# Optimization experiments

Hardware: AMD Instinct MI355X
Metric: run time of the kernel (lower is better)

## Reference

```python
import jax, jax.numpy as jnp
import numpy as np

N_NODES = 50000


def _graph_conv(x, src, dst, W, b):
    """DGL GraphConv with norm='both', bias, weight applied pre-aggregation.
    x: [N, Fin]; src/dst: [E] int; W: [Fin, Fout]; b: [Fout]."""
    N = x.shape[0]
    ones = jnp.ones(src.shape, jnp.float32)
    deg_out = jnp.maximum(jax.ops.segment_sum(ones, src, num_segments=N), 1.0)
    deg_in = jnp.maximum(jax.ops.segment_sum(ones, dst, num_segments=N), 1.0)
    h = (x * jax.lax.rsqrt(deg_out)[:, None]) @ W          # [N, Fout]
    m = jax.ops.segment_sum(h[src], dst, num_segments=N)   # SpMM aggregate
    return m * jax.lax.rsqrt(deg_in)[:, None] + b


def setup_inputs() -> dict:
    key = jax.random.key(0)
    ks = jax.random.split(key, 12)
    N = N_NODES
    e_sizes = {"rsr": 3000000, "rtr": 1000000, "rur": 200000}
    inp = {"x": jax.random.normal(ks[0], (N, 32), jnp.float32)}
    for i, (name, E) in enumerate(e_sizes.items()):
        inp[f"src_{name}"] = jax.random.randint(ks[1 + 2 * i], (E,), 0, N, jnp.int64)
        inp[f"dst_{name}"] = jax.random.randint(ks[2 + 2 * i], (E,), 0, N, jnp.int64)
    inp["W1"] = jax.random.normal(ks[7], (3, 32, 16), jnp.float32) / np.sqrt(32.0)
    inp["b1"] = jnp.zeros((3, 16), jnp.float32)
    inp["W2"] = jax.random.normal(ks[8], (3, 16, 1), jnp.float32) / np.sqrt(16.0)
    inp["b2"] = jnp.zeros((3, 1), jnp.float32)
    return inp


def reference(x, src_rsr, dst_rsr, src_rtr, dst_rtr, src_rur, dst_rur, W1, b1, W2, b2):
    edges = [(src_rsr, dst_rsr), (src_rtr, dst_rtr), (src_rur, dst_rur)]
    # layer 1: HeteroGraphConv(sum over relations) -> relu
    h = sum(_graph_conv(x, s, d, W1[r], b1[r]) for r, (s, d) in enumerate(edges))
    h = jax.nn.relu(h)
    # layer 2 -> squeeze
    out = sum(_graph_conv(h, s, d, W2[r], b2[r]) for r, (s, d) in enumerate(edges))
    return out[:, 0]
```

## Files before the change

### kernel.cpp

```cpp
#include <hip/hip_runtime.h>

#define N_NODES 50000
#define FH 16
#define NBUK 782
#define BSHIFT 6
#define BSTRIDE 800
#define TILE 4096
#define NCH2 64
#define NRNG 8
#define RNGSZ 6250
#define C1CAP 4608

#define OFF_INVOUT   0u
#define OFF_INVIN    150000u
#define OFF_BUKCNT   300000u
#define OFF_BSTART   302400u
#define OFF_GCUR     304800u
#define OFF_ROWPTR   307200u
#define OFF_HPROJ    457216u
#define OFF_HOUT     2857216u
#define OFF_AGGP     3657216u
#define OFF_SRCHIST  3657216u
#define OFF_HS       6057216u
#define OFF_OUTP     6207216u
#define OFF_PAIRS    6357216u
#define OFF_SRCSORT  10557216u

__global__ void k_zero_u32(unsigned* __restrict__ p, int n) {
    int i = blockIdx.x * 256 + threadIdx.x;
    if (i < n) p[i] = 0u;
}

__global__ __launch_bounds__(256) void k_srcDeg(const int* s0, const int* s1, const int* s2,
                                                int E0, int E1, int E2,
                                                unsigned* __restrict__ histP) {
    __shared__ unsigned bins[RNGSZ / 2];
    int c = blockIdx.x, rg = blockIdx.y, r = blockIdx.z;
    const int* arr = (r == 0) ? s0 : (r == 1) ? s1 : s2;
    int E = (r == 0) ? E0 : (r == 1) ? E1 : E2;
    for (int i = threadIdx.x; i < RNGSZ / 2; i += 256) bins[i] = 0u;
    __syncthreads();
    int lo = rg * RNGSZ;
    int per = (((E + NCH2 - 1) / NCH2) + 7) & ~7;
    int a0 = c * per, a1 = min(a0 + per, E);
    for (int i = a0 + (int)threadIdx.x * 8; i < a1; i += 2048) {
        if (i + 8 <= a1) {
            int4 v1 = *reinterpret_cast<const int4*>(arr + i);
            int4 v2 = *reinterpret_cast<const int4*>(arr + i + 4);
            unsigned d0 = (unsigned)(v1.x - lo), d1 = (unsigned)(v1.y - lo);
            unsigned d2 = (unsigned)(v1.z - lo), d3 = (unsigned)(v1.w - lo);
            unsigned d4 = (unsigned)(v2.x - lo), d5 = (unsigned)(v2.y - lo);
            unsigned d6 = (unsigned)(v2.z - lo), d7 = (unsigned)(v2.w - lo);
            if (d0 < (unsigned)RNGSZ) atomicAdd(&bins[d0 >> 1], (d0 & 1u) ? 65536u : 1u);
            if (d1 < (unsigned)RNGSZ) atomicAdd(&bins[d1 >> 1], (d1 & 1u) ? 65536u : 1u);
            if (d2 < (unsigned)RNGSZ) atomicAdd(&bins[d2 >> 1], (d2 & 1u) ? 65536u : 1u);
            if (d3 < (unsigned)RNGSZ) atomicAdd(&bins[d3 >> 1], (d3 & 1u) ? 65536u : 1u);
            if (d4 < (unsigned)RNGSZ) atomicAdd(&bins[d4 >> 1], (d4 & 1u) ? 65536u : 1u);
            if (d5 < (unsigned)RNGSZ) atomicAdd(&bins[d5 >> 1], (d5 & 1u) ? 65536u : 1u);
            if (d6 < (unsigned)RNGSZ) atomicAdd(&bins[d6 >> 1], (d6 & 1u) ? 65536u : 1u);
            if (d7 < (unsigned)RNGSZ) atomicAdd(&bins[d7 >> 1], (d7 & 1u) ? 65536u : 1u);
        } else {
            for (int k2 = i; k2 < a1; k2++) {
                unsigned d = (unsigned)(arr[k2] - lo);
                if (d < (unsigned)RNGSZ) atomicAdd(&bins[d >> 1], (d & 1u) ? 65536u : 1u);
            }
        }
    }
    __syncthreads();
    unsigned* out = histP + ((size_t)r * NCH2 + c) * 25000 + rg * (RNGSZ / 2);
    for (int i = threadIdx.x; i < RNGSZ / 2; i += 256) out[i] = bins[i];
}

__global__ void k_degreduceOut(const unsigned* __restrict__ histP, float* __restrict__ invOut) {
    int n = blockIdx.x * 256 + threadIdx.x;
    int r = blockIdx.y;
    if (n >= N_NODES) return;
    const unsigned* p = histP + (size_t)r * NCH2 * 25000 + (n >> 1);
    unsigned s = 0;
#pragma unroll
    for (int c = 0; c < NCH2; c++) {
        unsigned w = p[(size_t)c * 25000];
        s += (n & 1) ? (w >> 16) : (w & 0xFFFFu);
    }
    invOut[r * N_NODES + n] = rsqrtf((float)(s ? s : 1u));
}

__global__ __launch_bounds__(256) void k_bukCount(const int* d0p, const int* d1p, const int* d2p,
                                                  int E0, int E1, int E2,
                                                  unsigned* __restrict__ bukCnt) {
    __shared__ unsigned bins[NBUK];
    int c = blockIdx.x, r = blockIdx.y;
    const int* arr = (r == 0) ? d0p : (r == 1) ? d1p : d2p;
    int E = (r == 0) ? E0 : (r == 1) ? E1 : E2;
    for (int i = threadIdx.x; i < NBUK; i += 256) bins[i] = 0u;
    __syncthreads();
    int nb = gridDim.x;
    int per = (((E + nb - 1) / nb) + 3) & ~3;
    int a0 = c * per, a1 = min(a0 + per, E);
    for (int i = a0 + (int)threadIdx.x * 4; i < a1; i += 1024) {
        if (i + 4 <= a1) {
            int4 v = *reinterpret_cast<const int4*>(arr + i);
            atomicAdd(&bins[((unsigned)v.x) >> BSHIFT], 1u);
            atomicAdd(&bins[((unsigned)v.y) >> BSHIFT], 1u);
            atomicAdd(&bins[((unsigned)v.z) >> BSHIFT], 1u);
            atomicAdd(&bins[((unsigned)v.w) >> BSHIFT], 1u);
        } else {
            for (int k2 = i; k2 < a1; k2++)
                atomicAdd(&bins[((unsigned)arr[k2]) >> BSHIFT], 1u);
        }
    }
    __syncthreads();
    for (int b = threadIdx.x; b < NBUK; b += 256)
        if (bins[b]) atomicAdd(&bukCnt[r * BSTRIDE + b], bins[b]);
}

__global__ __launch_bounds__(256) void k_bucketScan(const unsigned* __restrict__ bukCnt,
                                                    unsigned* __restrict__ bstart,
                                                    unsigned* __restrict__ gcur) {
    __shared__ unsigned part[256];
    int r = blockIdx.x, t = threadIdx.x;
    unsigned loc[4]; unsigned s = 0;
#pragma unroll
    for (int k = 0; k < 4; k++) {
        int idx = 4 * t + k;
        loc[k] = (idx < NBUK) ? bukCnt[r * BSTRIDE + idx] : 0u;
        s += loc[k];
    }
    part[t] = s;
    __syncthreads();
    for (int d = 1; d < 256; d <<= 1) {
        unsigned v = (t >= d) ? part[t - d] : 0u;
        __syncthreads();
        part[t] += v;
        __syncthreads();
    }
    unsigned run = part[t] - s;
#pragma unroll
    for (int k = 0; k < 4; k++) {
        int idx = 4 * t + k;
        if (idx <= NBUK) { bstart[r * BSTRIDE + idx] = run; gcur[r * BSTRIDE + idx] = run; }
        run += loc[k];
    }
}

__global__ __launch_bounds__(256) void k_passB(
    const int* s0p, const int* s1p, const int* s2p,
    const int* d0p, const int* d1p, const int* d2p,
    int E0, int E1, int E2, int po0, int po1, int po2,
    unsigned* __restrict__ pairsAll, unsigned* __restrict__ gcurAll) {
    __shared__ unsigned cnt[NBUK];
    __shared__ unsigned off[NBUK];
    __shared__ unsigned gbase[NBUK];
    __shared__ unsigned part[256];
    __shared__ unsigned spair[TILE];
    __shared__ unsigned saddr[TILE];
    int r = blockIdx.z;
    const int* src = (r == 0) ? s0p : (r == 1) ? s1p : s2p;
    const int* dst = (r == 0) ? d0p : (r == 1) ? d1p : d2p;
    int E = (r == 0) ? E0 : (r == 1) ? E1 : E2;
    unsigned* pairs = pairsAll + ((r == 0) ? po0 : (r == 1) ? po1 : po2);
    unsigned* gcur = gcurAll + r * BSTRIDE;
    int nb = gridDim.x;
    int chunk = (((E + nb - 1) / nb) + 15) & ~15;
    int c0 = blockIdx.x * chunk;
    int c1 = min(c0 + chunk, E);
    for (int t0 = c0; t0 < c1; t0 += TILE) {
        int tn = min(TILE, c1 - t0);
        for (int i = threadIdx.x; i < NBUK; i += 256) cnt[i] = 0u;
        __syncthreads();
        unsigned pk[16], bk[16], sl[16];
        if (tn == TILE) {
            int base = t0 + (int)threadIdx.x * 16;
#pragma unroll
            for (int q = 0; q < 4; q++) {
                int4 vs = *reinterpret_cast<const int4*>(src + base + q * 4);
                int4 vd = *reinterpret_cast<const int4*>(dst + base + q * 4);
                pk[q * 4 + 0] = ((unsigned)vd.x << 16) | (unsigned)vs.x;
                pk[q * 4 + 1] = ((unsigned)vd.y << 16) | (unsigned)vs.y;
                pk[q * 4 + 2] = ((unsigned)vd.z << 16) | (unsigned)vs.z;
                pk[q * 4 + 3] = ((unsigned)vd.w << 16) | (unsigned)vs.w;
                bk[q * 4 + 0] = (unsigned)vd.x >> BSHIFT;
                bk[q * 4 + 1] = (unsigned)vd.y >> BSHIFT;
                bk[q * 4 + 2] = (unsigned)vd.z >> BSHIFT;
                bk[q * 4 + 3] = (unsigned)vd.w >> BSHIFT;
            }
#pragma unroll
            for (int k = 0; k < 16; k++) sl[k] = atomicAdd(&cnt[bk[k]], 1u);
        } else {
#pragma unroll
            for (int k = 0; k < 16; k++) {
                int ii = k * 256 + (int)threadIdx.x;
                bk[k] = 0xFFFFFFFFu;
                if (ii < tn) {
                    int i = t0 + ii;
                    unsigned s = (unsigned)src[i], d = (unsigned)dst[i];
                    pk[k] = (d << 16) | s;
                    unsigned b = d >> BSHIFT;
                    bk[k] = b;
                    sl[k] = atomicAdd(&cnt[b], 1u);
                }
            }
        }
        __syncthreads();
        {
            int t = threadIdx.x;
            unsigned loc[4]; unsigned sloc = 0;
#pragma unroll
            for (int k2 = 0; k2 < 4; k2++) {
                int idx = 4 * t + k2;
                loc[k2] = (idx < NBUK) ? cnt[idx] : 0u;
                sloc += loc[k2];
            }
            part[t] = sloc;
            __syncthreads();
            for (int d = 1; d < 256; d <<= 1) {
                unsigned v = (t >= d) ? part[t - d] : 0u;
                __syncthreads();
                part[t] += v;
                __syncthreads();
            }
            unsigned run = part[t] - sloc;
#pragma unroll
            for (int k2 = 0; k2 < 4; k2++) {
                int idx = 4 * t + k2;
                if (idx < NBUK) off[idx] = run;
                run += loc[k2];
            }
        }
        __syncthreads();
        for (int b = threadIdx.x; b < NBUK; b += 256) {
            unsigned c = cnt[b];
            if (c) gbase[b] = atomicAdd(&gcur[b], c);
        }
        __syncthreads();
        if (tn == TILE) {
#pragma unroll
            for (int k = 0; k < 16; k++) {
                unsigned idx = off[bk[k]] + sl[k];
                spair[idx] = pk[k];
                saddr[idx] = gbase[bk[k]] + sl[k];
            }
        } else {
#pragma unroll
            for (int k = 0; k < 16; k++) {
                if (bk[k] != 0xFFFFFFFFu) {
                    unsigned idx = off[bk[k]] + sl[k];
                    spair[idx] = pk[k];
                    saddr[idx] = gbase[bk[k]] + sl[k];
                }
            }
        }
        __syncthreads();
#pragma unroll
        for (int k = 0; k < 16; k++) {
            int ii = k * 256 + (int)threadIdx.x;
            if (ii < tn) pairs[saddr[ii]] = spair[ii];
        }
        __syncthreads();
    }
}

__global__ __launch_bounds__(256) void k_h1(const float* __restrict__ x, const float* __restrict__ invOut,
                                            const float* __restrict__ W1, float* __restrict__ hproj) {
    __shared__ float sW[32 * FH];
    __shared__ float sx[16][32];
    int r = blockIdx.y;
    const float* W = W1 + r * 32 * FH;
    int t = threadIdx.x;
    for (int i = t; i < 32 * FH; i += 256) sW[i] = W[i];
    int n0 = blockIdx.x * 16;
    for (int i = t; i < 16 * 32; i += 256) {
        int nn = i >> 5, kk = i & 31;
        int n = n0 + nn;
        sx[nn][kk] = (n < N_NODES) ? x[n * 32 + kk] : 0.0f;
    }
    __syncthreads();
    int nn = t >> 4, j = t & 15;
    int n = n0 + nn;
    if (n < N_NODES) {
        float s = 0.f;
#pragma unroll
        for (int k = 0; k < 32; k++) s += sx[nn][k] * sW[k * FH + j];
        hproj[((size_t)r * N_NODES + n) * FH + j] = s * invOut[r * N_NODES + n];
    }
}

__global__ __launch_bounds__(256) void k_passC1(
    const unsigned* __restrict__ pairsAll, int po1, int po2,
    const unsigned* __restrict__ bstartAll,
    const float4* __restrict__ h4All, float4* __restrict__ out4All,
    unsigned short* __restrict__ srcGAll, unsigned* __restrict__ rowptrAll,
    float* __restrict__ invInAll) {
    __shared__ unsigned cnt[64];
    __shared__ unsigned off[65];
    __shared__ unsigned cur[64];
    __shared__ unsigned short srcS[C1CAP];
    int b = blockIdx.x, t = threadIdx.x, r = blockIdx.z;
    int po = (r == 0) ? 0 : (r == 1) ? po1 : po2;
    const unsigned* pairs = pairsAll + po;
    const unsigned* bstart = bstartAll + r * BSTRIDE;
    const float4* h4 = h4All + (size_t)r * N_NODES * 4;
    float4* out4 = out4All + (size_t)r * N_NODES * 4;
    unsigned short* srcG = srcGAll + po;
    unsigned* rowptr = rowptrAll + (size_t)r * (N_NODES + 1);
    float* invIn = invInAll + (size_t)r * N_NODES;
    unsigned e0 = bstart[b], e1 = bstart[b + 1];
    if (e1 - e0 > (unsigned)C1CAP) e1 = e0 + (unsigned)C1CAP;
    int d0 = b << BSHIFT;
    if (t < 64) cnt[t] = 0u;
    __syncthreads();
    for (unsigned i = e0 + t; i < e1; i += 256)
        atomicAdd(&cnt[(pairs[i] >> 16) - (unsigned)d0], 1u);
    __syncthreads();
    if (t < 64) {
        unsigned cv = cnt[t];
        unsigned sc = cv;
#pragma unroll
        for (int d = 1; d < 64; d <<= 1) {
            unsigned v = __shfl_up(sc, d, 64);
            if (t >= d) sc += v;
        }
        off[t] = sc - cv;
        if (t == 63) off[64] = sc;
    }
    __syncthreads();
    if (t < 64) {
        cur[t] = off[t];
        int n = d0 + t;
        if (n < N_NODES) {
            rowptr[n] = (unsigned)po + e0 + off[t];
            unsigned dg = cnt[t];
            invIn[n] = rsqrtf((float)(dg ? dg : 1u));
        }
    }
    if (b == NBUK - 1 && t == 0) rowptr[N_NODES] = (unsigned)po + e1;
    __syncthreads();
    for (unsigned i = e0 + t; i < e1; i += 256) {
        unsigned p = pairs[i];
        unsigned d = (p >> 16) - (unsigned)d0;
        unsigned pos = atomicAdd(&cur[d], 1u);
        srcS[pos] = (unsigned short)(p & 0xFFFFu);
    }
    __syncthreads();
    {
        unsigned len = e1 - e0;
        for (unsigned i = t; i < len; i += 256) srcG[e0 + i] = srcS[i];
    }
    int unit = t >> 4, p = t & 15, k = p >> 2, fq = p & 3;
    for (int nd = unit; nd < 64; nd += 16) {
        unsigned o0 = off[nd], o1 = off[nd + 1];
        float ax = 0.f, ay = 0.f, az = 0.f, aw = 0.f;
        unsigned base = o0;
        for (; base + 8 <= o1; base += 8) {
            int s0 = srcS[base + k], s1 = srcS[base + 4 + k];
            float4 v0 = h4[(size_t)s0 * 4 + fq];
            float4 v1 = h4[(size_t)s1 * 4 + fq];
            ax += v0.x + v1.x; ay += v0.y + v1.y; az += v0.z + v1.z; aw += v0.w + v1.w;
        }
        for (; base < o1; base += 4) {
            unsigned idx = base + (unsigned)k;
            if (idx < o1) {
                int s = srcS[idx];
                float4 v = h4[(size_t)s * 4 + fq];
                ax += v.x; ay += v.y; az += v.z; aw += v.w;
            }
        }
        ax += __shfl_xor(ax, 4, 16); ay += __shfl_xor(ay, 4, 16);
        az += __shfl_xor(az, 4, 16); aw += __shfl_xor(aw, 4, 16);
        ax += __shfl_xor(ax, 8, 16); ay += __shfl_xor(ay, 8, 16);
        az += __shfl_xor(az, 8, 16); aw += __shfl_xor(aw, 8, 16);
        int n = d0 + nd;
        if (k == 0 && n < N_NODES) {
            unsigned dg = o1 - o0;
            float sc = rsqrtf((float)(dg ? dg : 1u));
            float4 res; res.x = ax * sc; res.y = ay * sc; res.z = az * sc; res.w = aw * sc;
            out4[(size_t)n * 4 + fq] = res;
        }
    }
}

__global__ void k_relu(const float* __restrict__ aggP, const float* __restrict__ b1,
                       float* __restrict__ hout) {
    int i = blockIdx.x * 256 + threadIdx.x;
    if (i >= N_NODES * FH) return;
    int j = i & 15;
    const size_t SL = (size_t)N_NODES * FH;
    float v = aggP[i] + aggP[SL + i] + aggP[2 * SL + i]
            + b1[j] + b1[FH + j] + b1[2 * FH + j];
    hout[i] = fmaxf(v, 0.f);
}

__global__ void k_h2(const float* __restrict__ hout, const float* __restrict__ invOut,
                     const float* __restrict__ W2, float* __restrict__ hs) {
    int n = blockIdx.x * 256 + threadIdx.x;
    int r = blockIdx.y;
    if (n >= N_NODES) return;
    const float4* hp = (const float4*)(hout + (size_t)n * FH);
    const float* w = W2 + r * FH;
    float s = 0.f;
#pragma unroll
    for (int q = 0; q < 4; q++) {
        float4 hv = hp[q];
        s += hv.x * w[q * 4 + 0] + hv.y * w[q * 4 + 1] + hv.z * w[q * 4 + 2] + hv.w * w[q * 4 + 3];
    }
    hs[r * N_NODES + n] = s * invOut[r * N_NODES + n];
}

__global__ __launch_bounds__(256) void k_passC2(
    const unsigned short* __restrict__ srcG, const unsigned* __restrict__ rowptr,
    const float* __restrict__ hsAll, const float* __restrict__ invIn,
    float* __restrict__ outP) {
    int t = threadIdx.x;
    int unit = t >> 4, p = t & 15;
    int gid = blockIdx.x * 16 + unit;
    if (gid >= 3 * N_NODES) return;
    int r = gid / N_NODES;
    int n = gid - r * N_NODES;
    unsigned o0 = rowptr[r * (N_NODES + 1) + n];
    unsigned o1 = rowptr[r * (N_NODES + 1) + n + 1];
    const float* hs = hsAll + (size_t)r * N_NODES;
    float s = 0.f;
    for (unsigned i = o0 + (unsigned)p; i < o1; i += 16) s += hs[srcG[i]];
    s += __shfl_xor(s, 1, 16); s += __shfl_xor(s, 2, 16);
    s += __shfl_xor(s, 4, 16); s += __shfl_xor(s, 8, 16);
    if (p == 0) outP[(size_t)r * N_NODES + n] = s * invIn[r * N_NODES + n];
}

__global__ void k_final(const float* __restrict__ outP, const float* __restrict__ b2,
                        float* __restrict__ out) {
    int n = blockIdx.x * 256 + threadIdx.x;
    if (n >= N_NODES) return;
    out[n] = outP[n] + outP[N_NODES + n] + outP[2 * (size_t)N_NODES + n]
           + b2[0] + b2[1] + b2[2];
}


__global__ void f_zero(float* __restrict__ p, int n) {
    int i = blockIdx.x * blockDim.x + threadIdx.x;
    if (i < n) p[i] = 0.0f;
}
__global__ void f_deg(const int* __restrict__ src, const int* __restrict__ dst, int E,
                      float* __restrict__ dout, float* __restrict__ din) {
    int i = blockIdx.x * blockDim.x + threadIdx.x;
    if (i < E) { atomicAdd(&dout[src[i]], 1.0f); atomicAdd(&din[dst[i]], 1.0f); }
}
__global__ void f_rsqrt(float* __restrict__ p, int n) {
    int i = blockIdx.x * blockDim.x + threadIdx.x;
    if (i < n) p[i] = rsqrtf(fmaxf(p[i], 1.0f));
}
__global__ void f_agg1(const int* __restrict__ src, const int* __restrict__ dst, int E,
                       const float* __restrict__ h, const float* __restrict__ invin,
                       float* __restrict__ agg) {
    int idx = blockIdx.x * blockDim.x + threadIdx.x;
    if (idx < E * FH) {
        int e = idx >> 4, j = idx & 15;
        atomicAdd(&agg[dst[e] * FH + j], h[src[e] * FH + j] * invin[dst[e]]);
    }
}
__global__ void f_relu(float* __restrict__ agg, const float* __restrict__ b1) {
    int i = blockIdx.x * blockDim.x + threadIdx.x;
    if (i < N_NODES * FH) {
        int j = i & 15;
        agg[i] = fmaxf(agg[i] + b1[j] + b1[FH + j] + b1[2 * FH + j], 0.0f);
    }
}
__global__ void f_outinit(float* __restrict__ out, const float* __restrict__ b2) {
    int i = blockIdx.x * blockDim.x + threadIdx.x;
    if (i < N_NODES) out[i] = b2[0] + b2[1] + b2[2];
}
__global__ void f_h2(const float* __restrict__ h1, const float* __restrict__ invout,
                     const float* __restrict__ W2r, float* __restrict__ hsv) {
    int n = blockIdx.x * blockDim.x + threadIdx.x;
    if (n < N_NODES) {
        const float4* hp = (const float4*)(h1 + (size_t)n * FH);
        float s = 0.0f;
#pragma unroll
        for (int q = 0; q < 4; q++) {
            float4 hv = hp[q];
            s += hv.x * W2r[q * 4] + hv.y * W2r[q * 4 + 1] + hv.z * W2r[q * 4 + 2] + hv.w * W2r[q * 4 + 3];
        }
        hsv[n] = s * invout[n];
    }
}
__global__ void f_agg2(const int* __restrict__ src, const int* __restrict__ dst, int E,
                       const float* __restrict__ hsv, const float* __restrict__ invin,
                       float* __restrict__ out) {
    int e = blockIdx.x * blockDim.x + threadIdx.x;
    if (e < E) atomicAdd(&out[dst[e]], hsv[src[e]] * invin[dst[e]]);
}


extern "C" void kernel_launch(void* const* d_in, const int* in_sizes, int n_in,
                              void* d_out, int out_size, void* d_ws, size_t ws_size,
                              hipStream_t stream) {
    const float* x = (const float*)d_in[0];
    const int* srcs[3] = { (const int*)d_in[1], (const int*)d_in[3], (const int*)d_in[5] };
    const int* dsts[3] = { (const int*)d_in[2], (const int*)d_in[4], (const int*)d_in[6] };
    int E[3] = { in_sizes[1], in_sizes[3], in_sizes[5] };
    const float* W1 = (const float*)d_in[7];
    const float* b1 = (const float*)d_in[8];
    const float* W2 = (const float*)d_in[9];
    const float* b2 = (const float*)d_in[10];
    float* out = (float*)d_out;
    const int N = N_NODES;
    const int B = 256;
    size_t Etot = (size_t)E[0] + E[1] + E[2];
    size_t need = ((size_t)OFF_SRCSORT + (Etot + 1) / 2) * 4u;

    if (ws_size >= need) {
        unsigned* ws = (unsigned*)d_ws;
        float* invOut = (float*)(ws + OFF_INVOUT);
        float* invIn  = (float*)(ws + OFF_INVIN);
        unsigned* bukCnt = ws + OFF_BUKCNT;
        unsigned* bstart = ws + OFF_BSTART;
        unsigned* gcur   = ws + OFF_GCUR;
        unsigned* rowptr = ws + OFF_ROWPTR;
        float* hproj = (float*)(ws + OFF_HPROJ);
        float* hout  = (float*)(ws + OFF_HOUT);
        float* aggP  = (float*)(ws + OFF_AGGP);
        unsigned* srcHist = ws + OFF_SRCHIST;
        float* hs    = (float*)(ws + OFF_HS);
        float* outP  = (float*)(ws + OFF_OUTP);
        unsigned* pairs = ws + OFF_PAIRS;
        unsigned short* srcSort = (unsigned short*)(ws + OFF_SRCSORT);
        int po[3] = { 0, E[0], E[0] + E[1] };

        k_zero_u32<<<(3 * BSTRIDE + B - 1) / B, B, 0, stream>>>(bukCnt, 3 * BSTRIDE);
        k_srcDeg<<<dim3(NCH2, NRNG, 3), B, 0, stream>>>(srcs[0], srcs[1], srcs[2],
                                                        E[0], E[1], E[2], srcHist);
        k_degreduceOut<<<dim3((N + B - 1) / B, 3), B, 0, stream>>>(srcHist, invOut);
        k_bukCount<<<dim3(256, 3), B, 0, stream>>>(dsts[0], dsts[1], dsts[2], E[0], E[1], E[2], bukCnt);
        k_bucketScan<<<3, B, 0, stream>>>(bukCnt, bstart, gcur);
        k_passB<<<dim3(256, 1, 3), B, 0, stream>>>(
            srcs[0], srcs[1], srcs[2], dsts[0], dsts[1], dsts[2],
            E[0], E[1], E[2], po[0], po[1], po[2], pairs, gcur);
        k_h1<<<dim3((N + 15) / 16, 3), B, 0, stream>>>(x, invOut, W1, hproj);
        k_passC1<<<dim3(NBUK, 1, 3), B, 0, stream>>>(
            pairs, po[1], po[2], bstart,
            (const float4*)hproj, (float4*)aggP,
            srcSort, rowptr, invIn);
        k_relu<<<(N * FH + B - 1) / B, B, 0, stream>>>(aggP, b1, hout);
        k_h2<<<dim3((N + B - 1) / B, 3), B, 0, stream>>>(hout, invOut, W2, hs);
        k_passC2<<<(3 * N + 15) / 16, B, 0, stream>>>(srcSort, rowptr, hs, invIn, outP);
        k_final<<<(N + B - 1) / B, B, 0, stream>>>(outP, b2, out);
    } else {
        float* wsf = (float*)d_ws;
        float* invOut = wsf;
        float* invIn = wsf + 3 * (size_t)N;
        float* h = wsf + 6 * (size_t)N;
        float* agg = wsf + 22 * (size_t)N;
        float* hsv = wsf + 38 * (size_t)N;
        f_zero<<<(6 * N + B - 1) / B, B, 0, stream>>>(invOut, 6 * N);
        f_zero<<<(16 * N + B - 1) / B, B, 0, stream>>>(agg, 16 * N);
        for (int r = 0; r < 3; r++)
            f_deg<<<(E[r] + B - 1) / B, B, 0, stream>>>(srcs[r], dsts[r], E[r],
                                                        invOut + (size_t)r * N, invIn + (size_t)r * N);
        f_rsqrt<<<(6 * N + B - 1) / B, B, 0, stream>>>(invOut, 6 * N);
        for (int r = 0; r < 3; r++) {
            k_h1<<<dim3((N + 15) / 16, 1), B, 0, stream>>>(x, invOut + (size_t)r * N,
                                                           W1 + (size_t)r * 32 * FH, h);
            f_agg1<<<(E[r] * FH + B - 1) / B, B, 0, stream>>>(srcs[r], dsts[r], E[r], h,
                                                              invIn + (size_t)r * N, agg);
        }
        f_relu<<<(N * FH + B - 1) / B, B, 0, stream>>>(agg, b1);
        f_outinit<<<(N + B - 1) / B, B, 0, stream>>>(out, b2);
        for (int r = 0; r < 3; r++) {
            f_h2<<<(N + B - 1) / B, B, 0, stream>>>(agg, invOut + (size_t)r * N,
                                                    W2 + (size_t)r * FH, hsv);
            f_agg2<<<(E[r] + B - 1) / B, B, 0, stream>>>(srcs[r], dsts[r], E[r], hsv,
                                                         invIn + (size_t)r * N, out);
        }
    }
}
```

Baseline: 243.7 us.

## Fuse small graph-conv kernels to cut launches and intermediate buffers

Folds the bucket-count zeroing into k_srcDeg, and merges the out-degree reduction and destination bucket counting into one k_misc launch whose block ranges do different jobs. It fuses relu and layer-2 projection into one kernel, so the hout buffer is never written or read back. The layer-2 aggregation now sums all three relations per node and adds the bias directly, which removes k_final and the outP buffer. This cuts four kernel launches and several global round trips, but it relies on the zeroing in block 0 of k_srcDeg finishing before k_misc runs, and passC2 now loops over relations serially inside each node unit.

```diff
diff --git a/kernel.cpp b/kernel.cpp
--- a/kernel.cpp
+++ b/kernel.cpp
@@ -18,24 +18,21 @@
 #define OFF_GCUR     304800u
 #define OFF_ROWPTR   307200u
 #define OFF_HPROJ    457216u
-#define OFF_HOUT     2857216u
 #define OFF_AGGP     3657216u
 #define OFF_SRCHIST  3657216u
 #define OFF_HS       6057216u
-#define OFF_OUTP     6207216u
 #define OFF_PAIRS    6357216u
 #define OFF_SRCSORT  10557216u
 
-__global__ void k_zero_u32(unsigned* __restrict__ p, int n) {
-    int i = blockIdx.x * 256 + threadIdx.x;
-    if (i < n) p[i] = 0u;
-}
-
 __global__ __launch_bounds__(256) void k_srcDeg(const int* s0, const int* s1, const int* s2,
                                                 int E0, int E1, int E2,
-                                                unsigned* __restrict__ histP) {
+                                                unsigned* __restrict__ histP,
+                                                unsigned* __restrict__ bukCnt) {
     __shared__ unsigned bins[RNGSZ / 2];
     int c = blockIdx.x, rg = blockIdx.y, r = blockIdx.z;
+    if (c == 0 && rg == 0 && r == 0) {
+        for (int i = threadIdx.x; i < 3 * BSTRIDE; i += 256) bukCnt[i] = 0u;
+    }
     const int* arr = (r == 0) ? s0 : (r == 1) ? s1 : s2;
     int E = (r == 0) ? E0 : (r == 1) ? E1 : E2;
     for (int i = threadIdx.x; i < RNGSZ / 2; i += 256) bins[i] = 0u;
@@ -71,31 +68,32 @@
     for (int i = threadIdx.x; i < RNGSZ / 2; i += 256) out[i] = bins[i];
 }
 
-__global__ void k_degreduceOut(const unsigned* __restrict__ histP, float* __restrict__ invOut) {
-    int n = blockIdx.x * 256 + threadIdx.x;
+__global__ __launch_bounds__(256) void k_misc(const unsigned* __restrict__ histP,
+                                              float* __restrict__ invOut,
+                                              const int* d0p, const int* d1p, const int* d2p,
+                                              int E0, int E1, int E2,
+                                              unsigned* __restrict__ bukCnt) {
+    __shared__ unsigned bins[NBUK];
     int r = blockIdx.y;
-    if (n >= N_NODES) return;
-    const unsigned* p = histP + (size_t)r * NCH2 * 25000 + (n >> 1);
-    unsigned s = 0;
-#pragma unroll
-    for (int c = 0; c < NCH2; c++) {
-        unsigned w = p[(size_t)c * 25000];
-        s += (n & 1) ? (w >> 16) : (w & 0xFFFFu);
-    }
-    invOut[r * N_NODES + n] = rsqrtf((float)(s ? s : 1u));
-}
-
-__global__ __launch_bounds__(256) void k_bukCount(const int* d0p, const int* d1p, const int* d2p,
-                                                  int E0, int E1, int E2,
-                                                  unsigned* __restrict__ bukCnt) {
-    __shared__ unsigned bins[NBUK];
-    int c = blockIdx.x, r = blockIdx.y;
+    if (blockIdx.x < 196) {
+        int n = blockIdx.x * 256 + threadIdx.x;
+        if (n >= N_NODES) return;
+        const unsigned* p = histP + (size_t)r * NCH2 * 25000 + (n >> 1);
+        unsigned s = 0;
+#pragma unroll
+        for (int c = 0; c < NCH2; c++) {
+            unsigned w = p[(size_t)c * 25000];
+            s += (n & 1) ? (w >> 16) : (w & 0xFFFFu);
+        }
+        invOut[r * N_NODES + n] = rsqrtf((float)(s ? s : 1u));
+        return;
+    }
+    int c = blockIdx.x - 196;
     const int* arr = (r == 0) ? d0p : (r == 1) ? d1p : d2p;
     int E = (r == 0) ? E0 : (r == 1) ? E1 : E2;
     for (int i = threadIdx.x; i < NBUK; i += 256) bins[i] = 0u;
     __syncthreads();
-    int nb = gridDim.x;
-    int per = (((E + nb - 1) / nb) + 3) & ~3;
+    int per = (((E + 255) / 256) + 3) & ~3;
     int a0 = c * per, a1 = min(a0 + per, E);
     for (int i = a0 + (int)threadIdx.x * 4; i < a1; i += 1024) {
         if (i + 4 <= a1) {
@@ -379,59 +377,61 @@
     }
 }
 
-__global__ void k_relu(const float* __restrict__ aggP, const float* __restrict__ b1,
-                       float* __restrict__ hout) {
-    int i = blockIdx.x * 256 + threadIdx.x;
-    if (i >= N_NODES * FH) return;
-    int j = i & 15;
-    const size_t SL = (size_t)N_NODES * FH;
-    float v = aggP[i] + aggP[SL + i] + aggP[2 * SL + i]
-            + b1[j] + b1[FH + j] + b1[2 * FH + j];
-    hout[i] = fmaxf(v, 0.f);
-}
-
-__global__ void k_h2(const float* __restrict__ hout, const float* __restrict__ invOut,
-                     const float* __restrict__ W2, float* __restrict__ hs) {
-    int n = blockIdx.x * 256 + threadIdx.x;
-    int r = blockIdx.y;
+__global__ __launch_bounds__(256) void k_relu_h2(const float4* __restrict__ aggP4,
+                                                 const float* __restrict__ invOut,
+                                                 const float* __restrict__ b1,
+                                                 const float* __restrict__ W2,
+                                                 float* __restrict__ hs) {
+    __shared__ float sW[3 * FH];
+    __shared__ float sb[FH];
+    int t = threadIdx.x;
+    if (t < 48) sW[t] = W2[t];
+    if (t < 16) sb[t] = b1[t] + b1[FH + t] + b1[2 * FH + t];
+    __syncthreads();
+    int n = blockIdx.x * 256 + t;
     if (n >= N_NODES) return;
-    const float4* hp = (const float4*)(hout + (size_t)n * FH);
-    const float* w = W2 + r * FH;
-    float s = 0.f;
+    const size_t SL4 = (size_t)N_NODES * 4;
+    float h[FH];
 #pragma unroll
     for (int q = 0; q < 4; q++) {
-        float4 hv = hp[q];
-        s += hv.x * w[q * 4 + 0] + hv.y * w[q * 4 + 1] + hv.z * w[q * 4 + 2] + hv.w * w[q * 4 + 3];
-    }
-    hs[r * N_NODES + n] = s * invOut[r * N_NODES + n];
-}
-
-__global__ __launch_bounds__(256) void k_passC2(
+        float4 a0 = aggP4[(size_t)n * 4 + q];
+        float4 a1 = aggP4[SL4 + (size_t)n * 4 + q];
+        float4 a2 = aggP4[2 * SL4 + (size_t)n * 4 + q];
+        h[q * 4 + 0] = fmaxf(a0.x + a1.x + a2.x + sb[q * 4 + 0], 0.f);
+        h[q * 4 + 1] = fmaxf(a0.y + a1.y + a2.y + sb[q * 4 + 1], 0.f);
+        h[q * 4 + 2] = fmaxf(a0.z + a1.z + a2.z + sb[q * 4 + 2], 0.f);
+        h[q * 4 + 3] = fmaxf(a0.w + a1.w + a2.w + sb[q * 4 + 3], 0.f);
+    }
+#pragma unroll
+    for (int r = 0; r < 3; r++) {
+        float s = 0.f;
+#pragma unroll
+        for (int j = 0; j < FH; j++) s += h[j] * sW[r * FH + j];
+        hs[r * N_NODES + n] = s * invOut[r * N_NODES + n];
+    }
+}
+
+__global__ __launch_bounds__(256) void k_passC2f(
     const unsigned short* __restrict__ srcG, const unsigned* __restrict__ rowptr,
     const float* __restrict__ hsAll, const float* __restrict__ invIn,
-    float* __restrict__ outP) {
+    const float* __restrict__ b2, float* __restrict__ out) {
     int t = threadIdx.x;
     int unit = t >> 4, p = t & 15;
-    int gid = blockIdx.x * 16 + unit;
-    if (gid >= 3 * N_NODES) return;
-    int r = gid / N_NODES;
-    int n = gid - r * N_NODES;
-    unsigned o0 = rowptr[r * (N_NODES + 1) + n];
-    unsigned o1 = rowptr[r * (N_NODES + 1) + n + 1];
-    const float* hs = hsAll + (size_t)r * N_NODES;
-    float s = 0.f;
-    for (unsigned i = o0 + (unsigned)p; i < o1; i += 16) s += hs[srcG[i]];
-    s += __shfl_xor(s, 1, 16); s += __shfl_xor(s, 2, 16);
-    s += __shfl_xor(s, 4, 16); s += __shfl_xor(s, 8, 16);
-    if (p == 0) outP[(size_t)r * N_NODES + n] = s * invIn[r * N_NODES + n];
-}
-
-__global__ void k_final(const float* __restrict__ outP, const float* __restrict__ b2,
-                        float* __restrict__ out) {
-    int n = blockIdx.x * 256 + threadIdx.x;
+    int n = blockIdx.x * 16 + unit;
     if (n >= N_NODES) return;
-    out[n] = outP[n] + outP[N_NODES + n] + outP[2 * (size_t)N_NODES + n]
-           + b2[0] + b2[1] + b2[2];
+    float tot = 0.f;
+#pragma unroll
+    for (int r = 0; r < 3; r++) {
+        unsigned o0 = rowptr[r * (N_NODES + 1) + n];
+        unsigned o1 = rowptr[r * (N_NODES + 1) + n + 1];
+        const float* hs = hsAll + (size_t)r * N_NODES;
+        float s = 0.f;
+        for (unsigned i = o0 + (unsigned)p; i < o1; i += 16) s += hs[srcG[i]];
+        tot += s * invIn[r * N_NODES + n];
+    }
+    tot += __shfl_xor(tot, 1, 16); tot += __shfl_xor(tot, 2, 16);
+    tot += __shfl_xor(tot, 4, 16); tot += __shfl_xor(tot, 8, 16);
+    if (p == 0) out[n] = tot + b2[0] + b2[1] + b2[2];
 }
 
 
@@ -516,20 +516,18 @@
         unsigned* gcur   = ws + OFF_GCUR;
         unsigned* rowptr = ws + OFF_ROWPTR;
         float* hproj = (float*)(ws + OFF_HPROJ);
-        float* hout  = (float*)(ws + OFF_HOUT);
         float* aggP  = (float*)(ws + OFF_AGGP);
         unsigned* srcHist = ws + OFF_SRCHIST;
         float* hs    = (float*)(ws + OFF_HS);
-        float* outP  = (float*)(ws + OFF_OUTP);
         unsigned* pairs = ws + OFF_PAIRS;
         unsigned short* srcSort = (unsigned short*)(ws + OFF_SRCSORT);
         int po[3] = { 0, E[0], E[0] + E[1] };
 
-        k_zero_u32<<<(3 * BSTRIDE + B - 1) / B, B, 0, stream>>>(bukCnt, 3 * BSTRIDE);
         k_srcDeg<<<dim3(NCH2, NRNG, 3), B, 0, stream>>>(srcs[0], srcs[1], srcs[2],
-                                                        E[0], E[1], E[2], srcHist);
-        k_degreduceOut<<<dim3((N + B - 1) / B, 3), B, 0, stream>>>(srcHist, invOut);
-        k_bukCount<<<dim3(256, 3), B, 0, stream>>>(dsts[0], dsts[1], dsts[2], E[0], E[1], E[2], bukCnt);
+                                                        E[0], E[1], E[2], srcHist, bukCnt);
+        k_misc<<<dim3(196 + 256, 3), B, 0, stream>>>(srcHist, invOut,
+                                                     dsts[0], dsts[1], dsts[2],
+                                                     E[0], E[1], E[2], bukCnt);
         k_bucketScan<<<3, B, 0, stream>>>(bukCnt, bstart, gcur);
         k_passB<<<dim3(256, 1, 3), B, 0, stream>>>(
             srcs[0], srcs[1], srcs[2], dsts[0], dsts[1], dsts[2],
@@ -539,10 +537,8 @@
             pairs, po[1], po[2], bstart,
             (const float4*)hproj, (float4*)aggP,
             srcSort, rowptr, invIn);
-        k_relu<<<(N * FH + B - 1) / B, B, 0, stream>>>(aggP, b1, hout);
-        k_h2<<<dim3((N + B - 1) / B, 3), B, 0, stream>>>(hout, invOut, W2, hs);
-        k_passC2<<<(3 * N + 15) / 16, B, 0, stream>>>(srcSort, rowptr, hs, invIn, outP);
-        k_final<<<(N + B - 1) / B, B, 0, stream>>>(outP, b2, out);
+        k_relu_h2<<<(N + B - 1) / B, B, 0, stream>>>((const float4*)aggP, invOut, b1, W2, hs);
+        k_passC2f<<<(N + 15) / 16, B, 0, stream>>>(srcSort, rowptr, hs, invIn, b2, out);
     } else {
         float* wsf = (float*)d_ws;
         float* invOut = wsf;
```

After: 242.6 us. About the same (-0.5%).
